# Performance work log

Hardware: AMD Instinct MI355X
Metric: run time of the kernel (lower is better)

## Reference

```python
import jax, jax.numpy as jnp
import numpy as np

N = 50000          # nodes
E = 1600000        # edges (avg degree 32)
DIMS = [128, 128, 128, 64]  # in_features + hidden_dims


def setup_inputs() -> dict:
    key = jax.random.key(0)
    ks = jax.random.split(key, 10)
    x = jax.random.normal(ks[0], (N, DIMS[0]), dtype=jnp.float32)
    edge_index = jax.random.randint(ks[1], (2, E), 0, N, dtype=jnp.int64)
    edge_weight = jax.random.uniform(ks[2], (E,), dtype=jnp.float32)
    params = {}
    for i in range(3):
        fan_in, fan_out = DIMS[i], DIMS[i + 1]
        scale = jnp.sqrt(6.0 / (fan_in + fan_out))  # glorot as in PyG GCNConv lin
        params[f"W{i+1}"] = jax.random.uniform(ks[3 + i], (fan_in, fan_out), jnp.float32, -scale, scale)
        params[f"b{i+1}"] = jnp.zeros((fan_out,), jnp.float32)
    return dict(x=x, edge_index=edge_index, edge_weight=edge_weight, **params)


def gcn_norm(edge_index, edge_weight, n):
    # PyG gcn_norm: add self-loops (weight 1), symmetric deg^-1/2 normalization
    src, dst = edge_index[0], edge_index[1]
    loop = jnp.arange(n, dtype=src.dtype)
    src = jnp.concatenate([src, loop])
    dst = jnp.concatenate([dst, loop])
    ew = jnp.concatenate([edge_weight, jnp.ones((n,), edge_weight.dtype)])
    deg = jax.ops.segment_sum(ew, dst, num_segments=n)  # degree at target
    dinv = jnp.where(deg > 0, jax.lax.rsqrt(jnp.maximum(deg, 1e-30)), 0.0)
    return src, dst, dinv[src] * ew * dinv[dst]


def gcn_conv(x, W, b, src, dst, norm, n):
    h = x @ W                                   # [N, out]
    msg = h[src] * norm[:, None]                # gather + edge scale
    agg = jax.ops.segment_sum(msg, dst, num_segments=n)  # scatter-add to targets
    return agg + b


def reference(x, edge_index, edge_weight, W1, b1, W2, b2, W3, b3):
    n = x.shape[0]
    src, dst, norm = gcn_norm(edge_index, edge_weight, n)
    x = jax.nn.relu(gcn_conv(x, W1, b1, src, dst, norm, n))
    x = jax.nn.relu(gcn_conv(x, W2, b2, src, dst, norm, n))
    return gcn_conv(x, W3, b3, src, dst, norm, n)
```

## Files before the change

kernel.cpp:

```cpp
#include <hip/hip_runtime.h>
#include <hip/hip_bf16.h>
#include <hip/hip_fp16.h>


#define K_IN 128
#define FIX_SCALE 8388608.0f
#define CE 4096

typedef _Float16 f16x8 __attribute__((ext_vector_type(8)));
typedef float f32x4 __attribute__((ext_vector_type(4)));

__global__ __launch_bounds__(1024) void part_count(const int* __restrict__ dst,
                                                   int* __restrict__ counts,
                                                   unsigned short* __restrict__ lrank,
                                                   int nb, int nblk, int e) {
    __shared__ int c[256];
    int t = threadIdx.x, blk = blockIdx.x;
    for (int i = t; i < nb; i += 1024) c[i] = 0;
    __syncthreads();
    int b0 = blk * CE;
#pragma unroll
    for (int j = 0; j < 4; j++) {
        int i = b0 + j * 1024 + t;
        if (i < e) {
            int b = dst[i] >> 8;
            int r = atomicAdd(&c[b], 1);
            lrank[i] = (unsigned short)r;
        }
    }
    __syncthreads();
    for (int i = t; i < nb; i += 1024) counts[(size_t)i * nblk + blk] = c[i];
}

__global__ __launch_bounds__(256) void reduce_kernel(const int* __restrict__ v,
                                                     int* __restrict__ bs, int m) {
    __shared__ int s[256];
    int t = threadIdx.x, i = blockIdx.x * 256 + t;
    s[t] = (i < m) ? v[i] : 0;
    __syncthreads();
    for (int off = 128; off > 0; off >>= 1) {
        if (t < off) s[t] += s[t + off];
        __syncthreads();
    }
    if (t == 0) bs[blockIdx.x] = s[0];
}

__global__ __launch_bounds__(1024) void scanb1024(const int* __restrict__ bs,
                                                  int* __restrict__ bo, int nbb) {
    __shared__ int s[1024];
    int t = threadIdx.x;
    s[t] = (t < nbb) ? bs[t] : 0;
    __syncthreads();
    for (int off = 1; off < 1024; off <<= 1) {
        int cur = s[t];
        int add = (t >= off) ? s[t - off] : 0;
        __syncthreads();
        s[t] = cur + add;
        __syncthreads();
    }
    if (t < nbb) bo[t] = (t == 0) ? 0 : s[t - 1];
}

__global__ __launch_bounds__(256) void scanw_kernel(const int* __restrict__ v,
                                                    const int* __restrict__ bo,
                                                    int* __restrict__ outp, int m) {
    __shared__ int s[256];
    int t = threadIdx.x, i = blockIdx.x * 256 + t;
    int c = (i < m) ? v[i] : 0;
    s[t] = c;
    __syncthreads();
    for (int off = 1; off < 256; off <<= 1) {
        int cur = s[t];
        int add = (t >= off) ? s[t - off] : 0;
        __syncthreads();
        s[t] = cur + add;
        __syncthreads();
    }
    if (i < m) outp[i] = bo[blockIdx.x] + (s[t] - c);
}

__global__ __launch_bounds__(1024) void part_scatter(const int* __restrict__ src,
                                                     const int* __restrict__ dst,
                                                     const float* __restrict__ ew,
                                                     const int* __restrict__ base,
                                                     const unsigned short* __restrict__ lrank,
                                                     int2* __restrict__ arr1,
                                                     unsigned char* __restrict__ dlow,
                                                     int nblk, int e) {
    int t = threadIdx.x, blk = blockIdx.x;
    int b0 = blk * CE;
#pragma unroll
    for (int j = 0; j < 4; j++) {
        int i = b0 + j * 1024 + t;
        if (i < e) {
            int d = dst[i];
            int b = d >> 8;
            int pos = base[(size_t)b * nblk + blk] + lrank[i];
            arr1[pos] = make_int2(src[i], __float_as_int(ew[i]));
            dlow[pos] = (unsigned char)(d & 255);
        }
    }
}

__global__ __launch_bounds__(1024) void bucket_csr(const int2* __restrict__ arr1,
                                                   const unsigned char* __restrict__ dlow,
                                                   const int* __restrict__ base,
                                                   unsigned short* __restrict__ rank2,
                                                   float* __restrict__ dinv,
                                                   int* __restrict__ row_ptr,
                                                   int2* __restrict__ ep,
                                                   int nb, int nblk, int n, int e) {
    __shared__ int cnt2[256];
    __shared__ unsigned int fxs[256];
    __shared__ int nbase[256];
    __shared__ float ldsdinv[256];
    __shared__ int ss[256];
    int t = threadIdx.x, b = blockIdx.x;
    int beg = base[(size_t)b * nblk];
    int end = (b + 1 < nb) ? base[(size_t)(b + 1) * nblk] : e;
    if (t < 256) { cnt2[t] = 0; fxs[t] = 0u; }
    __syncthreads();
    for (int i = beg + t; i < end; i += 1024) {
        int ld = dlow[i];
        int r = atomicAdd(&cnt2[ld], 1);
        rank2[i] = (unsigned short)r;
        float w = __int_as_float(arr1[i].y);
        atomicAdd(&fxs[ld], (unsigned int)(w * FIX_SCALE + 0.5f));
    }
    __syncthreads();
    if (t < 256) ss[t] = cnt2[t];
    __syncthreads();
    for (int off = 1; off < 256; off <<= 1) {
        int cur = 0, add = 0;
        if (t < 256) { cur = ss[t]; add = (t >= off) ? ss[t - off] : 0; }
        __syncthreads();
        if (t < 256) ss[t] = cur + add;
        __syncthreads();
    }
    if (t < 256) {
        nbase[t] = ss[t] - cnt2[t];
        int d = b * 256 + t;
        if (d < n) {
            float dv = rsqrtf(1.0f + (float)fxs[t] * (1.0f / FIX_SCALE));
            dinv[d] = dv;
            ldsdinv[t] = dv;
            row_ptr[d] = beg + nbase[t];
        }
    }
    __syncthreads();
    for (int i = beg + t; i < end; i += 1024) {
        int ld = dlow[i];
        int pos = beg + nbase[ld] + rank2[i];
        int2 a = arr1[i];
        float w = __int_as_float(a.y) * ldsdinv[ld];
        ep[pos] = make_int2(a.x, __float_as_int(w));
    }
}

__global__ void val_kernel(int2* __restrict__ ep, const float* __restrict__ dinv,
                           int* __restrict__ row_ptr, int n, int e) {
    int i = blockIdx.x * blockDim.x + threadIdx.x;
    if (i == 0) row_ptr[n] = e;
    if (i >= e) return;
    int2 a = ep[i];
    float w = __int_as_float(a.y) * dinv[a.x];
    ep[i] = make_int2(a.x << 8, __float_as_int(w));
}

__global__ void wt_prep_all(const float* __restrict__ W1, const float* __restrict__ W2,
                            const float* __restrict__ W3, _Float16* __restrict__ Wt1,
                            _Float16* __restrict__ Wt2, _Float16* __restrict__ Wt3) {
    int i = blockIdx.x * 256 + threadIdx.x;
    if (i < 128 * 128) {
        int k = i >> 7, nn = i & 127;
        Wt1[(size_t)nn * 128 + k] = (_Float16)W1[i];
        return;
    }
    int j = i - 128 * 128;
    if (j < 128 * 128) {
        int k = j >> 7, nn = j & 127;
        Wt2[(size_t)nn * 128 + k] = (_Float16)W2[j];
        return;
    }
    int l = j - 128 * 128;
    if (l < 64 * 128) {
        int k = l >> 6, nn = l & 63;
        Wt3[(size_t)nn * 128 + k] = (_Float16)W3[l];
    }
}

template <int NOUT, bool XF16>
__global__ __launch_bounds__(256) void mfma_gemm(const void* __restrict__ Xv,
                                                 const _Float16* __restrict__ Wt,
                                                 _Float16* __restrict__ H, int n) {
    constexpr int CTW = NOUT / 64;
    __shared__ _Float16 Xs[64][136];
    __shared__ _Float16 Ws[NOUT][136];
    int t = threadIdx.x;
    int row0 = blockIdx.x * 64;

    for (int i = t * 8; i < NOUT * K_IN; i += 2048) {
        int nn = i >> 7, k = i & 127;
        *(uint4*)&Ws[nn][k] = *(const uint4*)&Wt[i];
    }
    if (XF16) {
        const _Float16* X = (const _Float16*)Xv;
        for (int i = t * 8; i < 64 * K_IN; i += 2048) {
            int r = i >> 7, k = i & 127;
            int row = row0 + r;
            uint4 v = make_uint4(0u, 0u, 0u, 0u);
            if (row < n) v = *(const uint4*)(X + (size_t)row * K_IN + k);
            *(uint4*)&Xs[r][k] = v;
        }
    } else {
        const float* X = (const float*)Xv;
        for (int i = t * 4; i < 64 * K_IN; i += 1024) {
            int r = i >> 7, k = i & 127;
            int row = row0 + r;
            float4 x4 = make_float4(0.f, 0.f, 0.f, 0.f);
            if (row < n) x4 = *(const float4*)(X + (size_t)row * K_IN + k);
            union { _Float16 h[4]; uint2 u; } uu;
            uu.h[0] = (_Float16)x4.x; uu.h[1] = (_Float16)x4.y;
            uu.h[2] = (_Float16)x4.z; uu.h[3] = (_Float16)x4.w;
            *(uint2*)&Xs[r][k] = uu.u;
        }
    }
    __syncthreads();

    int lane = t & 63, w = t >> 6;
    int m = lane & 15, g = lane >> 4;
    f32x4 acc[4][CTW];
#pragma unroll
    for (int mt = 0; mt < 4; mt++)
#pragma unroll
        for (int ct = 0; ct < CTW; ct++) acc[mt][ct] = (f32x4){0.f, 0.f, 0.f, 0.f};

#pragma unroll
    for (int kt = 0; kt < 4; kt++) {
        int kb = kt * 32 + g * 8;
        f16x8 a[4];
#pragma unroll
        for (int mt = 0; mt < 4; mt++) a[mt] = *(const f16x8*)&Xs[mt * 16 + m][kb];
#pragma unroll
        for (int ct = 0; ct < CTW; ct++) {
            int nn = w * (16 * CTW) + ct * 16 + m;
            f16x8 b = *(const f16x8*)&Ws[nn][kb];
#pragma unroll
            for (int mt = 0; mt < 4; mt++)
                acc[mt][ct] = __builtin_amdgcn_mfma_f32_16x16x32_f16(a[mt], b, acc[mt][ct], 0, 0, 0);
        }
    }

#pragma unroll
    for (int mt = 0; mt < 4; mt++) {
#pragma unroll
        for (int r = 0; r < 4; r++) {
            int row = row0 + mt * 16 + g * 4 + r;
            if (row < n) {
#pragma unroll
                for (int ct = 0; ct < CTW; ct++)
                    H[(size_t)row * NOUT + w * (16 * CTW) + ct * 16 + m] =
                        (_Float16)acc[mt][ct][r];
            }
        }
    }
}

template <int F, bool RELU, bool OF16>
__global__ __launch_bounds__(256) void agg_kernel(const __half* __restrict__ H,
                                                  const int* __restrict__ row_ptr,
                                                  const int2* __restrict__ ep,
                                                  const float* __restrict__ dinv,
                                                  const float* __restrict__ bias,
                                                  void* __restrict__ outv, int n) {
    constexpr int UN = 16;
    int wid = threadIdx.x >> 6;
    int lane = threadIdx.x & 63;
    int node = blockIdx.x * 4 + wid;
    if (node >= n) return;

    int start = __builtin_amdgcn_readfirstlane(row_ptr[node]);
    int end   = __builtin_amdgcn_readfirstlane(row_ptr[node + 1]);
    float di = dinv[node];
    float sw = di * di;

    const unsigned lb = (unsigned)lane * (F == 128 ? 4u : 2u);

    float a0, a1;
    if (F == 128) {
        float2 s2 = __half22float2(((const __half2*)(H + (size_t)node * 128))[lane]);
        a0 = s2.x * sw; a1 = s2.y * sw;
    } else {
        a0 = __half2float(H[(size_t)node * 64 + lane]) * sw; a1 = 0.f;
    }

    int len = end - start;
    int nf = len / UN;
    for (int b = 0; b < nf; b++) {
        int p0 = start + b * UN;
        int2 e[UN];
#pragma unroll
        for (int u = 0; u < UN; u++) e[u] = ep[p0 + u];
        __half2 v2[UN];
        __half v1[UN];
#pragma unroll
        for (int u = 0; u < UN; u++) {
            unsigned off = (unsigned)e[u].x;
            if (F == 64) off >>= 1;
            if (F == 128) v2[u] = *(const __half2*)((const char*)H + (off + lb));
            else          v1[u] = *(const __half*)((const char*)H + (off + lb));
        }
#pragma unroll
        for (int u = 0; u < UN; u++) {
            float w = __int_as_float(e[u].y);
            if (F == 128) {
                float2 f = __half22float2(v2[u]);
                a0 += w * f.x; a1 += w * f.y;
            } else {
                a0 += w * __half2float(v1[u]);
            }
        }
    }
    int base = start + nf * UN;
    if (base < end) {
        int2 e[UN];
#pragma unroll
        for (int u = 0; u < UN; u++) {
            int p = base + u;
            int q = (p < end) ? p : end - 1;
            int2 t2 = ep[q];
            if (p >= end) t2.y = 0;
            e[u] = t2;
        }
        __half2 v2[UN];
        __half v1[UN];
#pragma unroll
        for (int u = 0; u < UN; u++) {
            unsigned off = (unsigned)e[u].x;
            if (F == 64) off >>= 1;
            if (F == 128) v2[u] = *(const __half2*)((const char*)H + (off + lb));
            else          v1[u] = *(const __half*)((const char*)H + (off + lb));
        }
#pragma unroll
        for (int u = 0; u < UN; u++) {
            float w = __int_as_float(e[u].y);
            if (F == 128) {
                float2 f = __half22float2(v2[u]);
                a0 += w * f.x; a1 += w * f.y;
            } else {
                a0 += w * __half2float(v1[u]);
            }
        }
    }

    if (F == 128) {
        float o0 = a0 + bias[lane * 2];
        float o1 = a1 + bias[lane * 2 + 1];
        if (RELU) { o0 = fmaxf(o0, 0.f); o1 = fmaxf(o1, 0.f); }
        if (OF16) {
            ((__half2*)outv)[(size_t)node * 64 + lane] = __floats2half2_rn(o0, o1);
        } else {
            *(float2*)((float*)outv + (size_t)node * 128 + lane * 2) = make_float2(o0, o1);
        }
    } else {
        float o = a0 + bias[lane];
        if (RELU) o = fmaxf(o, 0.f);
        if (OF16) ((__half*)outv)[(size_t)node * 64 + lane] = __float2half(o);
        else      ((float*)outv)[(size_t)node * 64 + lane] = o;
    }
}


extern "C" void kernel_launch(void* const* d_in, const int* in_sizes, int n_in,
                              void* d_out, int out_size, void* d_ws, size_t ws_size,
                              hipStream_t stream) {
    const float* x   = (const float*)d_in[0];
    const int*   ei  = (const int*)d_in[1];
    const float* ew  = (const float*)d_in[2];
    const float* W1  = (const float*)d_in[3];
    const float* b1  = (const float*)d_in[4];
    const float* W2  = (const float*)d_in[5];
    const float* b2  = (const float*)d_in[6];
    const float* W3  = (const float*)d_in[7];
    const float* b3  = (const float*)d_in[8];
    float* out = (float*)d_out;

    const int N = in_sizes[0] / K_IN;
    const int E = in_sizes[2];
    const int* src = ei;
    const int* dst = ei + E;

    const int NB   = (N + 255) >> 8;
    const int NBLK = (E + CE - 1) / CE;
    const int M    = NB * NBLK;
    const int NBB  = (M + 255) / 256;

    char* w = (char*)d_ws;
    auto alloc = [&](size_t bytes) {
        void* p = (void*)w;
        w += (bytes + 255) & ~(size_t)255;
        return p;
    };
    int*            counts = (int*)alloc((size_t)M * 4);
    int*            base   = (int*)alloc((size_t)M * 4);
    int*            bsM    = (int*)alloc((size_t)NBB * 4);
    int*            boM    = (int*)alloc((size_t)NBB * 4);
    unsigned short* lrank  = (unsigned short*)alloc((size_t)E * 2);
    int2*           arr1   = (int2*)alloc((size_t)E * 8);
    unsigned char*  dlow   = (unsigned char*)alloc((size_t)E);
    float*          dinv   = (float*)alloc((size_t)N * 4);
    int*            row_ptr= (int*)alloc((size_t)(N + 1) * 4);
    int2*           ep     = (int2*)alloc((size_t)E * 8);
    _Float16*       Wt1    = (_Float16*)alloc(128 * 128 * 2);
    _Float16*       Wt2    = (_Float16*)alloc(128 * 128 * 2);
    _Float16*       Wt3    = (_Float16*)alloc(64 * 128 * 2);
    _Float16*       bufH   = (_Float16*)alloc((size_t)N * 128 * 2);
    _Float16*       bufX   = (_Float16*)alloc((size_t)N * 128 * 2);

    part_count<<<NBLK, 1024, 0, stream>>>(dst, counts, lrank, NB, NBLK, E);
    reduce_kernel<<<NBB, 256, 0, stream>>>(counts, bsM, M);
    scanb1024<<<1, 1024, 0, stream>>>(bsM, boM, NBB);
    scanw_kernel<<<NBB, 256, 0, stream>>>(counts, boM, base, M);
    part_scatter<<<NBLK, 1024, 0, stream>>>(src, dst, ew, base, lrank, arr1, dlow, NBLK, E);
    bucket_csr<<<NB, 1024, 0, stream>>>(arr1, dlow, base, lrank, dinv, row_ptr, ep,
                                        NB, NBLK, N, E);
    val_kernel<<<(E + 255) / 256, 256, 0, stream>>>(ep, dinv, row_ptr, N, E);

    wt_prep_all<<<(2 * 128 * 128 + 64 * 128 + 255) / 256, 256, 0, stream>>>(
        W1, W2, W3, Wt1, Wt2, Wt3);

    int gGemm = (N + 63) / 64;
    int gAgg  = (N + 3) / 4;

    mfma_gemm<128, false><<<gGemm, 256, 0, stream>>>(x, Wt1, bufH, N);
    agg_kernel<128, true, true><<<gAgg, 256, 0, stream>>>((const __half*)bufH, row_ptr, ep,
                                                          dinv, b1, bufX, N);
    mfma_gemm<128, true><<<gGemm, 256, 0, stream>>>(bufX, Wt2, bufH, N);
    agg_kernel<128, true, true><<<gAgg, 256, 0, stream>>>((const __half*)bufH, row_ptr, ep,
                                                          dinv, b2, bufX, N);
    mfma_gemm<64, true><<<gGemm, 256, 0, stream>>>(bufX, Wt3, bufH, N);
    agg_kernel<64, false, false><<<gAgg, 256, 0, stream>>>((const __half*)bufH, row_ptr, ep,
                                                           dinv, b3, out, N);
}
```

Measured before the change: 316.6 us.

## Fuse preprocessing kernels, pack dst-low into src, merge LDS atomics, bump unroll

Weight transposition is folded into extra blocks of the partition-count kernel, and the val_kernel pass is folded into extra blocks of the first GEMM launch, cutting two launches. The low 8 bits of dst are packed into the src word of arr1, so the separate dlow byte array and its reads and writes go away. The per-bucket count and fixed-point weight sums become a single 64-bit LDS atomic. The aggregation unroll rises from 16 to 24. Risks: src<<8 overflows if node ids reach 2^23, the 64-bit LDS atomics may be slower than two 32-bit ones, and the larger unroll raises register pressure.

```diff
diff --git a/kernel.cpp b/kernel.cpp
--- a/kernel.cpp
+++ b/kernel.cpp
@@ -10,12 +10,29 @@
 typedef _Float16 f16x8 __attribute__((ext_vector_type(8)));
 typedef float f32x4 __attribute__((ext_vector_type(4)));
 
-__global__ __launch_bounds__(1024) void part_count(const int* __restrict__ dst,
-                                                   int* __restrict__ counts,
-                                                   unsigned short* __restrict__ lrank,
-                                                   int nb, int nblk, int e) {
+__global__ __launch_bounds__(1024) void part_count_wt(
+    const int* __restrict__ dst, int* __restrict__ counts,
+    unsigned short* __restrict__ lrank, int nb, int nblk, int e,
+    const float* __restrict__ W1, const float* __restrict__ W2,
+    const float* __restrict__ W3, _Float16* __restrict__ Wt1,
+    _Float16* __restrict__ Wt2, _Float16* __restrict__ Wt3) {
+    int blk = blockIdx.x;
+    if (blk >= nblk) {
+        int i = (blk - nblk) * 1024 + threadIdx.x;
+        if (i < 128 * 128) {
+            int k = i >> 7, nn = i & 127;
+            Wt1[(size_t)nn * 128 + k] = (_Float16)W1[i];
+        } else if (i < 2 * 128 * 128) {
+            int j = i - 128 * 128, k = j >> 7, nn = j & 127;
+            Wt2[(size_t)nn * 128 + k] = (_Float16)W2[j];
+        } else if (i < 2 * 128 * 128 + 64 * 128) {
+            int l = i - 2 * 128 * 128, k = l >> 6, nn = l & 63;
+            Wt3[(size_t)nn * 128 + k] = (_Float16)W3[l];
+        }
+        return;
+    }
     __shared__ int c[256];
-    int t = threadIdx.x, blk = blockIdx.x;
+    int t = threadIdx.x;
     for (int i = t; i < nb; i += 1024) c[i] = 0;
     __syncthreads();
     int b0 = blk * CE;
@@ -85,7 +102,6 @@
                                                      const int* __restrict__ base,
                                                      const unsigned short* __restrict__ lrank,
                                                      int2* __restrict__ arr1,
-                                                     unsigned char* __restrict__ dlow,
                                                      int nblk, int e) {
     int t = threadIdx.x, blk = blockIdx.x;
     int b0 = blk * CE;
@@ -96,39 +112,38 @@
             int d = dst[i];
             int b = d >> 8;
             int pos = base[(size_t)b * nblk + blk] + lrank[i];
-            arr1[pos] = make_int2(src[i], __float_as_int(ew[i]));
-            dlow[pos] = (unsigned char)(d & 255);
+            arr1[pos] = make_int2((src[i] << 8) | (d & 255), __float_as_int(ew[i]));
         }
     }
 }
 
 __global__ __launch_bounds__(1024) void bucket_csr(const int2* __restrict__ arr1,
-                                                   const unsigned char* __restrict__ dlow,
                                                    const int* __restrict__ base,
                                                    unsigned short* __restrict__ rank2,
                                                    float* __restrict__ dinv,
                                                    int* __restrict__ row_ptr,
                                                    int2* __restrict__ ep,
                                                    int nb, int nblk, int n, int e) {
-    __shared__ int cnt2[256];
-    __shared__ unsigned int fxs[256];
+    __shared__ unsigned long long pk[256];
     __shared__ int nbase[256];
     __shared__ float ldsdinv[256];
     __shared__ int ss[256];
     int t = threadIdx.x, b = blockIdx.x;
     int beg = base[(size_t)b * nblk];
     int end = (b + 1 < nb) ? base[(size_t)(b + 1) * nblk] : e;
-    if (t < 256) { cnt2[t] = 0; fxs[t] = 0u; }
+    if (t < 256) pk[t] = 0ULL;
     __syncthreads();
     for (int i = beg + t; i < end; i += 1024) {
-        int ld = dlow[i];
-        int r = atomicAdd(&cnt2[ld], 1);
-        rank2[i] = (unsigned short)r;
-        float w = __int_as_float(arr1[i].y);
-        atomicAdd(&fxs[ld], (unsigned int)(w * FIX_SCALE + 0.5f));
-    }
-    __syncthreads();
-    if (t < 256) ss[t] = cnt2[t];
+        int2 a = arr1[i];
+        int ld = a.x & 255;
+        float w = __int_as_float(a.y);
+        unsigned long long fx = (unsigned long long)(unsigned int)(w * FIX_SCALE + 0.5f);
+        unsigned long long old = atomicAdd(&pk[ld], (fx << 32) | 1ULL);
+        rank2[i] = (unsigned short)(old & 0xffffffffULL);
+    }
+    __syncthreads();
+    int cnt = (t < 256) ? (int)(pk[t] & 0xffffffffULL) : 0;
+    if (t < 256) ss[t] = cnt;
     __syncthreads();
     for (int off = 1; off < 256; off <<= 1) {
         int cur = 0, add = 0;
@@ -138,10 +153,10 @@
         __syncthreads();
     }
     if (t < 256) {
-        nbase[t] = ss[t] - cnt2[t];
+        nbase[t] = ss[t] - cnt;
         int d = b * 256 + t;
         if (d < n) {
-            float dv = rsqrtf(1.0f + (float)fxs[t] * (1.0f / FIX_SCALE));
+            float dv = rsqrtf(1.0f + (float)(unsigned int)(pk[t] >> 32) * (1.0f / FIX_SCALE));
             dinv[d] = dv;
             ldsdinv[t] = dv;
             row_ptr[d] = beg + nbase[t];
@@ -149,54 +164,36 @@
     }
     __syncthreads();
     for (int i = beg + t; i < end; i += 1024) {
-        int ld = dlow[i];
+        int2 a = arr1[i];
+        int ld = a.x & 255;
         int pos = beg + nbase[ld] + rank2[i];
-        int2 a = arr1[i];
         float w = __int_as_float(a.y) * ldsdinv[ld];
-        ep[pos] = make_int2(a.x, __float_as_int(w));
-    }
-}
-
-__global__ void val_kernel(int2* __restrict__ ep, const float* __restrict__ dinv,
-                           int* __restrict__ row_ptr, int n, int e) {
-    int i = blockIdx.x * blockDim.x + threadIdx.x;
-    if (i == 0) row_ptr[n] = e;
-    if (i >= e) return;
-    int2 a = ep[i];
-    float w = __int_as_float(a.y) * dinv[a.x];
-    ep[i] = make_int2(a.x << 8, __float_as_int(w));
-}
-
-__global__ void wt_prep_all(const float* __restrict__ W1, const float* __restrict__ W2,
-                            const float* __restrict__ W3, _Float16* __restrict__ Wt1,
-                            _Float16* __restrict__ Wt2, _Float16* __restrict__ Wt3) {
-    int i = blockIdx.x * 256 + threadIdx.x;
-    if (i < 128 * 128) {
-        int k = i >> 7, nn = i & 127;
-        Wt1[(size_t)nn * 128 + k] = (_Float16)W1[i];
-        return;
-    }
-    int j = i - 128 * 128;
-    if (j < 128 * 128) {
-        int k = j >> 7, nn = j & 127;
-        Wt2[(size_t)nn * 128 + k] = (_Float16)W2[j];
-        return;
-    }
-    int l = j - 128 * 128;
-    if (l < 64 * 128) {
-        int k = l >> 6, nn = l & 63;
-        Wt3[(size_t)nn * 128 + k] = (_Float16)W3[l];
-    }
-}
-
-template <int NOUT, bool XF16>
+        ep[pos] = make_int2(a.x >> 8, __float_as_int(w));
+    }
+}
+
+template <int NOUT, bool XF16, bool FUSEVAL>
 __global__ __launch_bounds__(256) void mfma_gemm(const void* __restrict__ Xv,
                                                  const _Float16* __restrict__ Wt,
-                                                 _Float16* __restrict__ H, int n) {
+                                                 _Float16* __restrict__ H, int n,
+                                                 int gGemm, int vblk,
+                                                 int2* __restrict__ ep,
+                                                 const float* __restrict__ dinv,
+                                                 int* __restrict__ row_ptr, int e) {
     constexpr int CTW = NOUT / 64;
     __shared__ _Float16 Xs[64][136];
     __shared__ _Float16 Ws[NOUT][136];
     int t = threadIdx.x;
+    if (FUSEVAL && (int)blockIdx.x >= gGemm) {
+        int vb = blockIdx.x - gGemm;
+        if (vb == 0 && t == 0) row_ptr[n] = e;
+        for (int i = vb * 256 + t; i < e; i += vblk * 256) {
+            int2 a = ep[i];
+            float w = __int_as_float(a.y) * dinv[a.x];
+            ep[i] = make_int2(a.x << 8, __float_as_int(w));
+        }
+        return;
+    }
     int row0 = blockIdx.x * 64;
 
     for (int i = t * 8; i < NOUT * K_IN; i += 2048) {
@@ -273,7 +270,7 @@
                                                   const float* __restrict__ dinv,
                                                   const float* __restrict__ bias,
                                                   void* __restrict__ outv, int n) {
-    constexpr int UN = 16;
+    constexpr int UN = 24;
     int wid = threadIdx.x >> 6;
     int lane = threadIdx.x & 63;
     int node = blockIdx.x * 4 + wid;
@@ -394,6 +391,8 @@
     const int NBLK = (E + CE - 1) / CE;
     const int M    = NB * NBLK;
     const int NBB  = (M + 255) / 256;
+    const int NWT  = (2 * 128 * 128 + 64 * 128 + 1023) / 1024;
+    const int VBLK = 1024;
 
     char* w = (char*)d_ws;
     auto alloc = [&](size_t bytes) {
@@ -407,7 +406,6 @@
     int*            boM    = (int*)alloc((size_t)NBB * 4);
     unsigned short* lrank  = (unsigned short*)alloc((size_t)E * 2);
     int2*           arr1   = (int2*)alloc((size_t)E * 8);
-    unsigned char*  dlow   = (unsigned char*)alloc((size_t)E);
     float*          dinv   = (float*)alloc((size_t)N * 4);
     int*            row_ptr= (int*)alloc((size_t)(N + 1) * 4);
     int2*           ep     = (int2*)alloc((size_t)E * 8);
@@ -417,28 +415,28 @@
     _Float16*       bufH   = (_Float16*)alloc((size_t)N * 128 * 2);
     _Float16*       bufX   = (_Float16*)alloc((size_t)N * 128 * 2);
 
-    part_count<<<NBLK, 1024, 0, stream>>>(dst, counts, lrank, NB, NBLK, E);
+    int gGemm = (N + 63) / 64;
+    int gAgg  = (N + 3) / 4;
+
+    part_count_wt<<<NBLK + NWT, 1024, 0, stream>>>(dst, counts, lrank, NB, NBLK, E,
+                                                   W1, W2, W3, Wt1, Wt2, Wt3);
     reduce_kernel<<<NBB, 256, 0, stream>>>(counts, bsM, M);
     scanb1024<<<1, 1024, 0, stream>>>(bsM, boM, NBB);
     scanw_kernel<<<NBB, 256, 0, stream>>>(counts, boM, base, M);
-    part_scatter<<<NBLK, 1024, 0, stream>>>(src, dst, ew, base, lrank, arr1, dlow, NBLK, E);
-    bucket_csr<<<NB, 1024, 0, stream>>>(arr1, dlow, base, lrank, dinv, row_ptr, ep,
+    part_scatter<<<NBLK, 1024, 0, stream>>>(src, dst, ew, base, lrank, arr1, NBLK, E);
+    bucket_csr<<<NB, 1024, 0, stream>>>(arr1, base, lrank, dinv, row_ptr, ep,
                                         NB, NBLK, N, E);
-    val_kernel<<<(E + 255) / 256, 256, 0, stream>>>(ep, dinv, row_ptr, N, E);
-
-    wt_prep_all<<<(2 * 128 * 128 + 64 * 128 + 255) / 256, 256, 0, stream>>>(
-        W1, W2, W3, Wt1, Wt2, Wt3);
-
-    int gGemm = (N + 63) / 64;
-    int gAgg  = (N + 3) / 4;
-
-    mfma_gemm<128, false><<<gGemm, 256, 0, stream>>>(x, Wt1, bufH, N);
+
+    mfma_gemm<128, false, true><<<gGemm + VBLK, 256, 0, stream>>>(
+        x, Wt1, bufH, N, gGemm, VBLK, ep, dinv, row_ptr, E);
     agg_kernel<128, true, true><<<gAgg, 256, 0, stream>>>((const __half*)bufH, row_ptr, ep,
                                                           dinv, b1, bufX, N);
-    mfma_gemm<128, true><<<gGemm, 256, 0, stream>>>(bufX, Wt2, bufH, N);
+    mfma_gemm<128, true, false><<<gGemm, 256, 0, stream>>>(
+        bufX, Wt2, bufH, N, gGemm, 0, nullptr, nullptr, nullptr, 0);
     agg_kernel<128, true, true><<<gAgg, 256, 0, stream>>>((const __half*)bufH, row_ptr, ep,
                                                           dinv, b2, bufX, N);
-    mfma_gemm<64, true><<<gGemm, 256, 0, stream>>>(bufX, Wt3, bufH, N);
+    mfma_gemm<64, true, false><<<gGemm, 256, 0, stream>>>(
+        bufX, Wt3, bufH, N, gGemm, 0, nullptr, nullptr, nullptr, 0);
     agg_kernel<64, false, false><<<gAgg, 256, 0, stream>>>((const __half*)bufH, row_ptr, ep,
                                                            dinv, b3, out, N);
 }
```

After: 311.4 us. No clear change (-1.7%).
